# Kernel tuning notes

Hardware: AMD Instinct MI355X
Metric: run time of the kernel (lower is better)

## Reference

```python
import jax, jax.numpy as jnp
import numpy as np

HIDDEN = 3584
N_HEADS = 28
N_KV = 4
HEAD_DIM = HIDDEN // N_HEADS  # 128
BS, SEQ = 4, 2048
EPS = 1e-6
ROPE_THETA = 1000000.0


def setup_inputs() -> dict:
    key = jax.random.key(0)
    ks = jax.random.split(key, 9)
    s = 0.02
    x = jax.random.normal(ks[0], (BS, SEQ, HIDDEN), dtype=jnp.float32)
    positions = jnp.broadcast_to(jnp.arange(SEQ, dtype=jnp.int32), (BS, SEQ))
    ln_w = jnp.ones((HIDDEN,), dtype=jnp.float32)
    Wq = jax.random.normal(ks[1], (N_HEADS * HEAD_DIM, HIDDEN), dtype=jnp.float32) * s
    bq = jax.random.normal(ks[2], (N_HEADS * HEAD_DIM,), dtype=jnp.float32) * s
    Wk = jax.random.normal(ks[3], (N_KV * HEAD_DIM, HIDDEN), dtype=jnp.float32) * s
    bk = jax.random.normal(ks[4], (N_KV * HEAD_DIM,), dtype=jnp.float32) * s
    Wv = jax.random.normal(ks[5], (N_KV * HEAD_DIM, HIDDEN), dtype=jnp.float32) * s
    bv = jax.random.normal(ks[6], (N_KV * HEAD_DIM,), dtype=jnp.float32) * s
    Wo = jax.random.normal(ks[7], (HIDDEN, N_HEADS * HEAD_DIM), dtype=jnp.float32) * s
    return {"x": x, "positions": positions, "ln_w": ln_w, "Wq": Wq, "bq": bq,
            "Wk": Wk, "bk": bk, "Wv": Wv, "bv": bv, "Wo": Wo}


def _rms_norm(x, w, eps):
    var = jnp.mean(x * x, axis=-1, keepdims=True)
    return x * jax.lax.rsqrt(var + eps) * w


def _rope(x, positions):
    # x: [b, s, h, d], neox-style rotary, theta = ROPE_THETA
    d = x.shape[-1]
    inv_freq = 1.0 / (ROPE_THETA ** (jnp.arange(0, d, 2, dtype=jnp.float32) / d))
    ang = positions.astype(jnp.float32)[..., None] * inv_freq  # [b, s, d/2]
    cos = jnp.cos(ang)[:, :, None, :]
    sin = jnp.sin(ang)[:, :, None, :]
    x1, x2 = jnp.split(x, 2, axis=-1)
    return jnp.concatenate([x1 * cos - x2 * sin, x2 * cos + x1 * sin], axis=-1)


def reference(x, positions, ln_w, Wq, bq, Wk, bk, Wv, bv, Wo):
    bs, seq, _ = x.shape
    h = _rms_norm(x, ln_w, EPS)
    q = jnp.einsum('bsh,oh->bso', h, Wq) + bq
    k = jnp.einsum('bsh,oh->bso', h, Wk) + bk
    v = jnp.einsum('bsh,oh->bso', h, Wv) + bv  # computed but unused downstream (as in source)
    q = _rope(q.reshape(bs, seq, N_HEADS, HEAD_DIM), positions)
    k = _rope(k.reshape(bs, seq, N_KV, HEAD_DIM), positions)  # unused downstream (as in source)
    out = jnp.einsum('bso,ho->bsh', q.reshape(bs, seq, -1), Wo) + x
    return out
```

## Files before the change

kernel.cpp:

```cpp
#include <hip/hip_runtime.h>
#include <hip/hip_bf16.h>


#define HIDDEN   3584
#define NQ       3584
#define NTOK     8192
#define NPAIR    64
#define EPSV     1e-6f

typedef __hip_bfloat16 bf16;
typedef __bf16 bf16x8 __attribute__((ext_vector_type(8)));
typedef float  f32x4  __attribute__((ext_vector_type(4)));

static __device__ __forceinline__ unsigned short f2bu(float f) {
  bf16 h = __float2bfloat16(f);
  return __builtin_bit_cast(unsigned short, h);
}
static __device__ __forceinline__ void stv(float* p, float v) { *p = v; }
static __device__ __forceinline__ void stv(bf16* p, float v) { *p = __float2bfloat16(v); }

__global__ __launch_bounds__(256)
void cvt_f32_bf16(const float* __restrict__ s, bf16* __restrict__ d, int n4) {
  int i = blockIdx.x * 256 + threadIdx.x;
  if (i >= n4) return;
  float4 f = ((const float4*)s)[i];
  ushort4 o;
  o.x = f2bu(f.x); o.y = f2bu(f.y); o.z = f2bu(f.z); o.w = f2bu(f.w);
  ((ushort4*)d)[i] = o;
}

__global__ __launch_bounds__(256)
void rmsnorm_k(const float* __restrict__ x, const float* __restrict__ w,
               bf16* __restrict__ h) {
  const int row = blockIdx.x;
  const int t = threadIdx.x;
  const float4* xr = (const float4*)(x + (size_t)row * HIDDEN);
  const float4* wr = (const float4*)w;

  float4 v0 = xr[t], v1 = xr[t + 256], v2 = xr[t + 512];
  float4 v3 = make_float4(0.f, 0.f, 0.f, 0.f);
  if (t < 128) v3 = xr[t + 768];

  float ss = v0.x*v0.x + v0.y*v0.y + v0.z*v0.z + v0.w*v0.w
           + v1.x*v1.x + v1.y*v1.y + v1.z*v1.z + v1.w*v1.w
           + v2.x*v2.x + v2.y*v2.y + v2.z*v2.z + v2.w*v2.w
           + v3.x*v3.x + v3.y*v3.y + v3.z*v3.z + v3.w*v3.w;

#pragma unroll
  for (int off = 32; off > 0; off >>= 1) ss += __shfl_down(ss, off);
  __shared__ float red[4];
  if ((t & 63) == 0) red[t >> 6] = ss;
  __syncthreads();
  float tot = red[0] + red[1] + red[2] + red[3];
  float scale = rsqrtf(tot * (1.0f / HIDDEN) + EPSV);

  ushort4* hr = (ushort4*)(h + (size_t)row * HIDDEN);
  float4 w0 = wr[t], w1 = wr[t + 256], w2 = wr[t + 512];
  ushort4 o;
  o.x = f2bu(v0.x*scale*w0.x); o.y = f2bu(v0.y*scale*w0.y);
  o.z = f2bu(v0.z*scale*w0.z); o.w = f2bu(v0.w*scale*w0.w);
  hr[t] = o;
  o.x = f2bu(v1.x*scale*w1.x); o.y = f2bu(v1.y*scale*w1.y);
  o.z = f2bu(v1.z*scale*w1.z); o.w = f2bu(v1.w*scale*w1.w);
  hr[t + 256] = o;
  o.x = f2bu(v2.x*scale*w2.x); o.y = f2bu(v2.y*scale*w2.y);
  o.z = f2bu(v2.z*scale*w2.z); o.w = f2bu(v2.w*scale*w2.w);
  hr[t + 512] = o;
  if (t < 128) {
    float4 w3 = wr[t + 768];
    o.x = f2bu(v3.x*scale*w3.x); o.y = f2bu(v3.y*scale*w3.y);
    o.z = f2bu(v3.z*scale*w3.z); o.w = f2bu(v3.w*scale*w3.w);
    hr[t + 768] = o;
  }
}

__global__ __launch_bounds__(256)
void rope_tab_k(const int* __restrict__ pos, float2* __restrict__ tab) {
  int idx = blockIdx.x * 256 + threadIdx.x;
  int t = idx >> 6;
  int i = idx & 63;
  float inv = exp2f(-(float)i * (19.931568569324174f / 64.0f));
  float ang = (float)pos[t] * inv;
  float s, c;
  sincosf(ang, &s, &c);
  tab[idx] = make_float2(c, s);
}

__global__ __launch_bounds__(256)
void rope_apply_k(bf16* __restrict__ q, const float2* __restrict__ tab) {
  const int t = blockIdx.x;
  bf16* qt = q + (size_t)t * NQ;
  const float2* tb = tab + (size_t)t * NPAIR;
  for (int j = threadIdx.x; j < 28 * NPAIR; j += 256) {
    int head = j >> 6;
    int i = j & 63;
    float2 cs = tb[i];
    int base = head * 128 + i;
    float x1 = __bfloat162float(qt[base]);
    float x2 = __bfloat162float(qt[base + 64]);
    qt[base]      = __float2bfloat16(x1 * cs.x - x2 * cs.y);
    qt[base + 64] = __float2bfloat16(x2 * cs.x + x1 * cs.y);
  }
}

#define BMT 256
#define BNT 256
#define BKT 64

#define BARRIER() __builtin_amdgcn_s_barrier()
#define VMW(n)    asm volatile("s_waitcnt vmcnt(" #n ")" ::: "memory")

template <int MODE, typename OutT>
__global__ __launch_bounds__(512, 2)
void gemm256(const bf16* __restrict__ A, const bf16* __restrict__ B,
             const float* __restrict__ aux, OutT* __restrict__ C,
             int M, int N, int K) {
  __shared__ __align__(16) bf16 sA[2][BMT][BKT];
  __shared__ __align__(16) bf16 sB[2][BNT][BKT];

  const int tid  = threadIdx.x;
  const int wave = tid >> 6;
  const int lane = tid & 63;
  const int wm   = wave >> 2;
  const int wn   = wave & 3;
  const int fr   = lane & 15;
  const int ks   = lane >> 4;
  const int sx   = fr & 7;

  const int nwg = gridDim.x;
  const int cpx = nwg >> 3;
  const int swz = (blockIdx.x & 7) * cpx + (blockIdx.x >> 3);
  const int gn  = N / BNT;
  const int bm  = (swz / gn) * BMT;
  const int bn  = (swz % gn) * BNT;

  const bf16* Ab = A + (size_t)bm * K;
  const bf16* Bb = B + (size_t)bn * K;

  const int NT = K / BKT;

  const int srw = lane >> 3;
  const int ssl = lane & 7;

  auto stage64 = [&](const bf16* gpanel, int kt, bf16* ldst, int rbase) {
    const int r  = rbase + wave * 8 + srw;
    const int sg = ssl ^ srw;
    const bf16* src = gpanel + (size_t)r * K + (size_t)kt * BKT + sg * 8;
    __builtin_amdgcn_global_load_lds(
        (const __attribute__((address_space(1))) void*)src,
        (__attribute__((address_space(3))) void*)(ldst + (size_t)(wave * 8) * BKT),
        16, 0, 0);
  };
  auto stage16k = [&](int kind, int buf, int kt) {
    if (kt >= NT) return;
    if (kind == 0)      { stage64(Ab, kt, &sA[buf][0][0],   0);   stage64(Ab, kt, &sA[buf][128][0], 128); }
    else if (kind == 1) { stage64(Ab, kt, &sA[buf][64][0],  64);  stage64(Ab, kt, &sA[buf][192][0], 192); }
    else if (kind == 2) { stage64(Bb, kt, &sB[buf][0][0],   0);   stage64(Bb, kt, &sB[buf][64][0],  64); }
    else                { stage64(Bb, kt, &sB[buf][128][0], 128); stage64(Bb, kt, &sB[buf][192][0], 192); }
  };

  f32x4 acc[8][4];
#pragma unroll
  for (int i = 0; i < 8; ++i)
#pragma unroll
    for (int j = 0; j < 4; ++j)
      acc[i][j] = (f32x4){0.f, 0.f, 0.f, 0.f};

  bf16x8 bfr[4][2];
  bf16x8 afr[2][2];

  auto loadA = [&](int buf, int qq) {
#pragma unroll
    for (int i = 0; i < 2; ++i)
#pragma unroll
      for (int kk = 0; kk < 2; ++kk) {
        const int R  = wm * 128 + qq * 32 + i * 16 + fr;
        const int sp = (kk * 4 + ks) ^ sx;
        afr[i][kk] = *(const bf16x8*)&sA[buf][R][sp * 8];
      }
  };
  auto loadB = [&](int buf) {
#pragma unroll
    for (int j = 0; j < 4; ++j)
#pragma unroll
      for (int kk = 0; kk < 2; ++kk) {
        const int R  = wn * 64 + j * 16 + fr;
        const int sp = (kk * 4 + ks) ^ sx;
        bfr[j][kk] = *(const bf16x8*)&sB[buf][R][sp * 8];
      }
  };
  auto domfma = [&](int q) {
#pragma unroll
    for (int i = 0; i < 2; ++i)
#pragma unroll
      for (int j = 0; j < 4; ++j)
#pragma unroll
        for (int kk = 0; kk < 2; ++kk)
          acc[q * 2 + i][j] = __builtin_amdgcn_mfma_f32_16x16x32_bf16(
              afr[i][kk], bfr[j][kk], acc[q * 2 + i][j], 0, 0, 0);
  };

  stage16k(2, 0, 0); stage16k(3, 0, 0); stage16k(0, 0, 0); stage16k(1, 0, 0);
  stage16k(2, 1, 1); stage16k(3, 1, 1); stage16k(0, 1, 1);
  VMW(6);
  BARRIER();

  const int nit = NT / 2;

  for (int it = 0; it < nit; ++it) {
    const bool last = (it == nit - 1);
#pragma unroll
    for (int u = 0; u < 2; ++u) {
#pragma unroll
      for (int q = 0; q < 4; ++q) {
        const int ph = u * 4 + q;
        loadA(u, q);
        if (q == 0) loadB(u);
        if (ph == 0)      stage16k(1, 1, 2 * it + 1);
        else if (ph == 1) stage16k(2, 0, 2 * it + 2);
        else if (ph == 2) stage16k(3, 0, 2 * it + 2);
        else if (ph == 3) stage16k(0, 0, 2 * it + 2);
        else if (ph == 4) stage16k(1, 0, 2 * it + 2);
        else if (ph == 5) stage16k(2, 1, 2 * it + 3);
        else if (ph == 6) stage16k(3, 1, 2 * it + 3);
        else              stage16k(0, 1, 2 * it + 3);
        BARRIER();
        __builtin_amdgcn_s_setprio(1);
        domfma(q);
        __builtin_amdgcn_s_setprio(0);
        if (ph == 3) {
          if (!last) { VMW(6); } else { VMW(2); }
        } else if (ph == 5) {
          if (last)  { VMW(0); }
        } else if (ph == 7) {
          if (!last) { VMW(6); }
        }
        BARRIER();
      }
    }
  }

#pragma unroll
  for (int f = 0; f < 8; ++f) {
    const int rb = bm + wm * 128 + f * 16 + ks * 4;
#pragma unroll
    for (int j = 0; j < 4; ++j) {
      const int col = bn + wn * 64 + j * 16 + fr;
#pragma unroll
      for (int r = 0; r < 4; ++r) {
        const int row = rb + r;
        float v = acc[f][j][r];
        if (MODE == 0) v += aux[col];
        else           v += aux[(size_t)row * N + col];
        stv(&C[(size_t)row * N + col], v);
      }
    }
  }
}

extern "C" void kernel_launch(void* const* d_in, const int* in_sizes, int n_in,
                              void* d_out, int out_size, void* d_ws, size_t ws_size,
                              hipStream_t stream) {
  (void)in_sizes; (void)n_in; (void)out_size; (void)ws_size;
  const float* x    = (const float*)d_in[0];
  const int*   pos  = (const int*)d_in[1];
  const float* ln_w = (const float*)d_in[2];
  const float* Wq   = (const float*)d_in[3];
  const float* bq   = (const float*)d_in[4];
  const float* Wo   = (const float*)d_in[9];
  float* out = (float*)d_out;

  char* ws = (char*)d_ws;
  size_t off = 0;
  bf16* h    = (bf16*)(ws + off); off += (size_t)NTOK * HIDDEN * sizeof(bf16);
  bf16* q    = (bf16*)(ws + off); off += (size_t)NTOK * NQ * sizeof(bf16);
  bf16* Wqb  = (bf16*)(ws + off); off += (size_t)NQ * HIDDEN * sizeof(bf16);
  bf16* Wob  = (bf16*)(ws + off); off += (size_t)HIDDEN * NQ * sizeof(bf16);
  float2* tab = (float2*)(ws + off); off += (size_t)NTOK * NPAIR * sizeof(float2);

  const int n4 = NQ * HIDDEN / 4;
  cvt_f32_bf16<<<(n4 + 255) / 256, 256, 0, stream>>>(Wq, Wqb, n4);
  cvt_f32_bf16<<<(n4 + 255) / 256, 256, 0, stream>>>(Wo, Wob, n4);
  rmsnorm_k<<<NTOK, 256, 0, stream>>>(x, ln_w, h);
  rope_tab_k<<<(NTOK * NPAIR) / 256, 256, 0, stream>>>(pos, tab);

  const int nblk = (NTOK / BMT) * (NQ / BNT);
  gemm256<0, bf16><<<nblk, 512, 0, stream>>>(h, Wqb, bq, q, NTOK, NQ, HIDDEN);
  rope_apply_k<<<NTOK, 256, 0, stream>>>(q, tab);
  gemm256<1, float><<<nblk, 512, 0, stream>>>(q, Wob, x, out, NTOK, HIDDEN, NQ);
}
```

Before: 496.3 us.

## Load GEMM B operand straight from global into double-buffered registers, drop LDS B

Measured after the change: 742.1 us. 49.5% more time.

```diff
diff --git a/kernel.cpp b/kernel.cpp
--- a/kernel.cpp
+++ b/kernel.cpp
@@ -116,7 +116,6 @@
              const float* __restrict__ aux, OutT* __restrict__ C,
              int M, int N, int K) {
   __shared__ __align__(16) bf16 sA[2][BMT][BKT];
-  __shared__ __align__(16) bf16 sB[2][BNT][BKT];
 
   const int tid  = threadIdx.x;
   const int wave = tid >> 6;
@@ -142,22 +141,18 @@
   const int srw = lane >> 3;
   const int ssl = lane & 7;
 
-  auto stage64 = [&](const bf16* gpanel, int kt, bf16* ldst, int rbase) {
+  auto stage64 = [&](int kt, int buf, int rbase) {
+    if (kt >= NT) return;
     const int r  = rbase + wave * 8 + srw;
     const int sg = ssl ^ srw;
-    const bf16* src = gpanel + (size_t)r * K + (size_t)kt * BKT + sg * 8;
+    const bf16* src = Ab + (size_t)r * K + (size_t)kt * BKT + sg * 8;
     __builtin_amdgcn_global_load_lds(
         (const __attribute__((address_space(1))) void*)src,
-        (__attribute__((address_space(3))) void*)(ldst + (size_t)(wave * 8) * BKT),
+        (__attribute__((address_space(3))) void*)(&sA[buf][rbase][0] + (size_t)(wave * 8) * BKT),
         16, 0, 0);
   };
-  auto stage16k = [&](int kind, int buf, int kt) {
-    if (kt >= NT) return;
-    if (kind == 0)      { stage64(Ab, kt, &sA[buf][0][0],   0);   stage64(Ab, kt, &sA[buf][128][0], 128); }
-    else if (kind == 1) { stage64(Ab, kt, &sA[buf][64][0],  64);  stage64(Ab, kt, &sA[buf][192][0], 192); }
-    else if (kind == 2) { stage64(Bb, kt, &sB[buf][0][0],   0);   stage64(Bb, kt, &sB[buf][64][0],  64); }
-    else                { stage64(Bb, kt, &sB[buf][128][0], 128); stage64(Bb, kt, &sB[buf][192][0], 192); }
-  };
+  auto stageAH0 = [&](int kt, int buf) { stage64(kt, buf, 0);  stage64(kt, buf, 128); };
+  auto stageAH1 = [&](int kt, int buf) { stage64(kt, buf, 64); stage64(kt, buf, 192); };
 
   f32x4 acc[8][4];
 #pragma unroll
@@ -166,8 +161,21 @@
     for (int j = 0; j < 4; ++j)
       acc[i][j] = (f32x4){0.f, 0.f, 0.f, 0.f};
 
-  bf16x8 bfr[4][2];
+  bf16x8 bP[4][2], bN[4][2];
   bf16x8 afr[2][2];
+
+  auto loadBg = [&](int kt, bf16x8 (&dst)[4][2]) {
+    if (kt >= NT) return;
+#pragma unroll
+    for (int jf = 0; jf < 4; ++jf)
+#pragma unroll
+      for (int kk = 0; kk < 2; ++kk) {
+        const bf16* src = Bb + (size_t)(wn * 64 + jf * 16 + fr) * K
+                             + (size_t)kt * BKT + kk * 32 + ks * 8;
+        asm volatile("global_load_dwordx4 %0, %1, off"
+                     : "=v"(dst[jf][kk]) : "v"(src) : "memory");
+      }
+  };
 
   auto loadA = [&](int buf, int qq) {
 #pragma unroll
@@ -179,17 +187,7 @@
         afr[i][kk] = *(const bf16x8*)&sA[buf][R][sp * 8];
       }
   };
-  auto loadB = [&](int buf) {
-#pragma unroll
-    for (int j = 0; j < 4; ++j)
-#pragma unroll
-      for (int kk = 0; kk < 2; ++kk) {
-        const int R  = wn * 64 + j * 16 + fr;
-        const int sp = (kk * 4 + ks) ^ sx;
-        bfr[j][kk] = *(const bf16x8*)&sB[buf][R][sp * 8];
-      }
-  };
-  auto domfma = [&](int q) {
+  auto domfma = [&](int q, bf16x8 (&bc)[4][2]) {
 #pragma unroll
     for (int i = 0; i < 2; ++i)
 #pragma unroll
@@ -197,12 +195,13 @@
 #pragma unroll
         for (int kk = 0; kk < 2; ++kk)
           acc[q * 2 + i][j] = __builtin_amdgcn_mfma_f32_16x16x32_bf16(
-              afr[i][kk], bfr[j][kk], acc[q * 2 + i][j], 0, 0, 0);
-  };
-
-  stage16k(2, 0, 0); stage16k(3, 0, 0); stage16k(0, 0, 0); stage16k(1, 0, 0);
-  stage16k(2, 1, 1); stage16k(3, 1, 1); stage16k(0, 1, 1);
-  VMW(6);
+              afr[i][kk], bc[j][kk], acc[q * 2 + i][j], 0, 0, 0);
+  };
+
+  loadBg(0, bP);
+  stageAH0(0, 0); stageAH1(0, 0); stageAH0(1, 1);
+  VMW(2);
+  __builtin_amdgcn_sched_barrier(0);
   BARRIER();
 
   const int nit = NT / 2;
@@ -211,29 +210,22 @@
     const bool last = (it == nit - 1);
 #pragma unroll
     for (int u = 0; u < 2; ++u) {
+      const int kt = 2 * it + u;
 #pragma unroll
       for (int q = 0; q < 4; ++q) {
-        const int ph = u * 4 + q;
         loadA(u, q);
-        if (q == 0) loadB(u);
-        if (ph == 0)      stage16k(1, 1, 2 * it + 1);
-        else if (ph == 1) stage16k(2, 0, 2 * it + 2);
-        else if (ph == 2) stage16k(3, 0, 2 * it + 2);
-        else if (ph == 3) stage16k(0, 0, 2 * it + 2);
-        else if (ph == 4) stage16k(1, 0, 2 * it + 2);
-        else if (ph == 5) stage16k(2, 1, 2 * it + 3);
-        else if (ph == 6) stage16k(3, 1, 2 * it + 3);
-        else              stage16k(0, 1, 2 * it + 3);
+        if (q == 0)      stageAH1(kt + 1, u ^ 1);
+        else if (q == 1) { if (u == 0) loadBg(kt + 1, bN);
+                           else        loadBg(kt + 1, bP); }
+        else if (q == 2) stageAH0(kt + 2, u);
         BARRIER();
         __builtin_amdgcn_s_setprio(1);
-        domfma(q);
+        if (u == 0) domfma(q, bP);
+        else        domfma(q, bN);
         __builtin_amdgcn_s_setprio(0);
-        if (ph == 3) {
-          if (!last) { VMW(6); } else { VMW(2); }
-        } else if (ph == 5) {
-          if (last)  { VMW(0); }
-        } else if (ph == 7) {
-          if (!last) { VMW(6); }
+        if (q == 3) {
+          if (!last) { VMW(2); } else { VMW(0); }
+          __builtin_amdgcn_sched_barrier(0);
         }
         BARRIER();
       }
```

## Shrink GEMM tiles to 128x128 with simpler double-buffered pipeline

Applied to the files above, without the earlier changes.

Result: slower. 595.7 us (+20.0%).

```diff
diff --git a/kernel.cpp b/kernel.cpp
--- a/kernel.cpp
+++ b/kernel.cpp
@@ -103,16 +103,16 @@
   }
 }
 
-#define BMT 256
-#define BNT 256
+#define BMT 128
+#define BNT 128
 #define BKT 64
 
 #define BARRIER() __builtin_amdgcn_s_barrier()
 #define VMW(n)    asm volatile("s_waitcnt vmcnt(" #n ")" ::: "memory")
 
 template <int MODE, typename OutT>
-__global__ __launch_bounds__(512, 2)
-void gemm256(const bf16* __restrict__ A, const bf16* __restrict__ B,
+__global__ __launch_bounds__(512, 4)
+void gemm128(const bf16* __restrict__ A, const bf16* __restrict__ B,
              const float* __restrict__ aux, OutT* __restrict__ C,
              int M, int N, int K) {
   __shared__ __align__(16) bf16 sA[2][BMT][BKT];
@@ -143,116 +143,105 @@
   const int ssl = lane & 7;
 
   auto stage64 = [&](const bf16* gpanel, int kt, bf16* ldst, int rbase) {
+    if (kt >= NT) return;
     const int r  = rbase + wave * 8 + srw;
     const int sg = ssl ^ srw;
     const bf16* src = gpanel + (size_t)r * K + (size_t)kt * BKT + sg * 8;
     __builtin_amdgcn_global_load_lds(
         (const __attribute__((address_space(1))) void*)src,
-        (__attribute__((address_space(3))) void*)(ldst + (size_t)(wave * 8) * BKT),
+        (__attribute__((address_space(3))) void*)(ldst + (size_t)(rbase + wave * 8) * BKT),
         16, 0, 0);
   };
-  auto stage16k = [&](int kind, int buf, int kt) {
-    if (kt >= NT) return;
-    if (kind == 0)      { stage64(Ab, kt, &sA[buf][0][0],   0);   stage64(Ab, kt, &sA[buf][128][0], 128); }
-    else if (kind == 1) { stage64(Ab, kt, &sA[buf][64][0],  64);  stage64(Ab, kt, &sA[buf][192][0], 192); }
-    else if (kind == 2) { stage64(Bb, kt, &sB[buf][0][0],   0);   stage64(Bb, kt, &sB[buf][64][0],  64); }
-    else                { stage64(Bb, kt, &sB[buf][128][0], 128); stage64(Bb, kt, &sB[buf][192][0], 192); }
-  };
-
-  f32x4 acc[8][4];
-#pragma unroll
-  for (int i = 0; i < 8; ++i)
-#pragma unroll
-    for (int j = 0; j < 4; ++j)
+
+  f32x4 acc[4][2];
+#pragma unroll
+  for (int i = 0; i < 4; ++i)
+#pragma unroll
+    for (int j = 0; j < 2; ++j)
       acc[i][j] = (f32x4){0.f, 0.f, 0.f, 0.f};
 
-  bf16x8 bfr[4][2];
+  bf16x8 bfr[2][2];
   bf16x8 afr[2][2];
 
-  auto loadA = [&](int buf, int qq) {
+  auto loadA = [&](int buf, int half) {
 #pragma unroll
     for (int i = 0; i < 2; ++i)
 #pragma unroll
       for (int kk = 0; kk < 2; ++kk) {
-        const int R  = wm * 128 + qq * 32 + i * 16 + fr;
+        const int R  = half * 64 + wm * 32 + i * 16 + fr;
         const int sp = (kk * 4 + ks) ^ sx;
         afr[i][kk] = *(const bf16x8*)&sA[buf][R][sp * 8];
       }
   };
   auto loadB = [&](int buf) {
 #pragma unroll
-    for (int j = 0; j < 4; ++j)
+    for (int j = 0; j < 2; ++j)
 #pragma unroll
       for (int kk = 0; kk < 2; ++kk) {
-        const int R  = wn * 64 + j * 16 + fr;
+        const int R  = wn * 32 + j * 16 + fr;
         const int sp = (kk * 4 + ks) ^ sx;
         bfr[j][kk] = *(const bf16x8*)&sB[buf][R][sp * 8];
       }
   };
-  auto domfma = [&](int q) {
+  auto domfma = [&](int half) {
 #pragma unroll
     for (int i = 0; i < 2; ++i)
 #pragma unroll
-      for (int j = 0; j < 4; ++j)
+      for (int j = 0; j < 2; ++j)
 #pragma unroll
         for (int kk = 0; kk < 2; ++kk)
-          acc[q * 2 + i][j] = __builtin_amdgcn_mfma_f32_16x16x32_bf16(
-              afr[i][kk], bfr[j][kk], acc[q * 2 + i][j], 0, 0, 0);
-  };
-
-  stage16k(2, 0, 0); stage16k(3, 0, 0); stage16k(0, 0, 0); stage16k(1, 0, 0);
-  stage16k(2, 1, 1); stage16k(3, 1, 1); stage16k(0, 1, 1);
-  VMW(6);
+          acc[half * 2 + i][j] = __builtin_amdgcn_mfma_f32_16x16x32_bf16(
+              afr[i][kk], bfr[j][kk], acc[half * 2 + i][j], 0, 0, 0);
+  };
+
+  stage64(Bb, 0, &sB[0][0][0], 0);  stage64(Bb, 0, &sB[0][0][0], 64);
+  stage64(Ab, 0, &sA[0][0][0], 0);  stage64(Ab, 0, &sA[0][0][0], 64);
+  VMW(0);
   BARRIER();
 
-  const int nit = NT / 2;
-
-  for (int it = 0; it < nit; ++it) {
-    const bool last = (it == nit - 1);
+  for (int it = 0; it < NT / 2; ++it) {
 #pragma unroll
     for (int u = 0; u < 2; ++u) {
-#pragma unroll
-      for (int q = 0; q < 4; ++q) {
-        const int ph = u * 4 + q;
-        loadA(u, q);
-        if (q == 0) loadB(u);
-        if (ph == 0)      stage16k(1, 1, 2 * it + 1);
-        else if (ph == 1) stage16k(2, 0, 2 * it + 2);
-        else if (ph == 2) stage16k(3, 0, 2 * it + 2);
-        else if (ph == 3) stage16k(0, 0, 2 * it + 2);
-        else if (ph == 4) stage16k(1, 0, 2 * it + 2);
-        else if (ph == 5) stage16k(2, 1, 2 * it + 3);
-        else if (ph == 6) stage16k(3, 1, 2 * it + 3);
-        else              stage16k(0, 1, 2 * it + 3);
-        BARRIER();
-        __builtin_amdgcn_s_setprio(1);
-        domfma(q);
-        __builtin_amdgcn_s_setprio(0);
-        if (ph == 3) {
-          if (!last) { VMW(6); } else { VMW(2); }
-        } else if (ph == 5) {
-          if (last)  { VMW(0); }
-        } else if (ph == 7) {
-          if (!last) { VMW(6); }
+      const int kt = 2 * it + u;
+      const bool lastt = (kt == NT - 1);
+      loadA(u, 0);
+      loadB(u);
+      stage64(Bb, kt + 1, &sB[u ^ 1][0][0], 0);
+      stage64(Bb, kt + 1, &sB[u ^ 1][0][0], 64);
+      stage64(Ab, kt + 1, &sA[u ^ 1][0][0], 0);
+      BARRIER();
+      __builtin_amdgcn_s_setprio(1);
+      domfma(0);
+      __builtin_amdgcn_s_setprio(0);
+      if (lastt) { VMW(0); } else { VMW(3); }
+      BARRIER();
+      loadA(u, 1);
+      stage64(Ab, kt + 1, &sA[u ^ 1][0][0], 64);
+      BARRIER();
+      __builtin_amdgcn_s_setprio(1);
+      domfma(1);
+      __builtin_amdgcn_s_setprio(0);
+      if (lastt) { VMW(0); } else { VMW(1); }
+      BARRIER();
+    }
+  }
+
+#pragma unroll
+  for (int half = 0; half < 2; ++half) {
+#pragma unroll
+    for (int i = 0; i < 2; ++i) {
+      const int rb = bm + half * 64 + wm * 32 + i * 16 + ks * 4;
+#pragma unroll
+      for (int j = 0; j < 2; ++j) {
+        const int col = bn + wn * 32 + j * 16 + fr;
+#pragma unroll
+        for (int r = 0; r < 4; ++r) {
+          const int row = rb + r;
+          float v = acc[half * 2 + i][j][r];
+          if (MODE == 0) v += aux[col];
+          else           v += aux[(size_t)row * N + col];
+          stv(&C[(size_t)row * N + col], v);
         }
-        BARRIER();
-      }
-    }
-  }
-
-#pragma unroll
-  for (int f = 0; f < 8; ++f) {
-    const int rb = bm + wm * 128 + f * 16 + ks * 4;
-#pragma unroll
-    for (int j = 0; j < 4; ++j) {
-      const int col = bn + wn * 64 + j * 16 + fr;
-#pragma unroll
-      for (int r = 0; r < 4; ++r) {
-        const int row = rb + r;
-        float v = acc[f][j][r];
-        if (MODE == 0) v += aux[col];
-        else           v += aux[(size_t)row * N + col];
-        stv(&C[(size_t)row * N + col], v);
       }
     }
   }
@@ -285,7 +274,7 @@
   rope_tab_k<<<(NTOK * NPAIR) / 256, 256, 0, stream>>>(pos, tab);
 
   const int nblk = (NTOK / BMT) * (NQ / BNT);
-  gemm256<0, bf16><<<nblk, 512, 0, stream>>>(h, Wqb, bq, q, NTOK, NQ, HIDDEN);
+  gemm128<0, bf16><<<nblk, 512, 0, stream>>>(h, Wqb, bq, q, NTOK, NQ, HIDDEN);
   rope_apply_k<<<NTOK, 256, 0, stream>>>(q, tab);
-  gemm256<1, float><<<nblk, 512, 0, stream>>>(q, Wob, x, out, NTOK, HIDDEN, NQ);
-}
+  gemm128<1, float><<<nblk, 512, 0, stream>>>(q, Wob, x, out, NTOK, HIDDEN, NQ);
+}
```

## Fuse RoPE into Q-projection GEMM epilogue and merge weight conversions

Applied to the files above, without the earlier changes.

New measurement: 485.5 us. 2.2% less time.

```diff
diff --git a/kernel.cpp b/kernel.cpp
--- a/kernel.cpp
+++ b/kernel.cpp
@@ -20,9 +20,13 @@
 static __device__ __forceinline__ void stv(bf16* p, float v) { *p = __float2bfloat16(v); }
 
 __global__ __launch_bounds__(256)
-void cvt_f32_bf16(const float* __restrict__ s, bf16* __restrict__ d, int n4) {
+void cvt2_f32_bf16(const float* __restrict__ s1, bf16* __restrict__ d1,
+                   const float* __restrict__ s2, bf16* __restrict__ d2, int n4) {
   int i = blockIdx.x * 256 + threadIdx.x;
-  if (i >= n4) return;
+  const float* s; bf16* d;
+  if (i < n4)           { s = s1; d = d1; }
+  else if (i < 2 * n4)  { s = s2; d = d2; i -= n4; }
+  else return;
   float4 f = ((const float4*)s)[i];
   ushort4 o;
   o.x = f2bu(f.x); o.y = f2bu(f.y); o.z = f2bu(f.z); o.w = f2bu(f.w);
@@ -86,23 +90,6 @@
   tab[idx] = make_float2(c, s);
 }
 
-__global__ __launch_bounds__(256)
-void rope_apply_k(bf16* __restrict__ q, const float2* __restrict__ tab) {
-  const int t = blockIdx.x;
-  bf16* qt = q + (size_t)t * NQ;
-  const float2* tb = tab + (size_t)t * NPAIR;
-  for (int j = threadIdx.x; j < 28 * NPAIR; j += 256) {
-    int head = j >> 6;
-    int i = j & 63;
-    float2 cs = tb[i];
-    int base = head * 128 + i;
-    float x1 = __bfloat162float(qt[base]);
-    float x2 = __bfloat162float(qt[base + 64]);
-    qt[base]      = __float2bfloat16(x1 * cs.x - x2 * cs.y);
-    qt[base + 64] = __float2bfloat16(x2 * cs.x + x1 * cs.y);
-  }
-}
-
 #define BMT 256
 #define BNT 256
 #define BKT 64
@@ -113,8 +100,8 @@
 template <int MODE, typename OutT>
 __global__ __launch_bounds__(512, 2)
 void gemm256(const bf16* __restrict__ A, const bf16* __restrict__ B,
-             const float* __restrict__ aux, OutT* __restrict__ C,
-             int M, int N, int K) {
+             const float* __restrict__ aux, const float2* __restrict__ tab,
+             OutT* __restrict__ C, int M, int N, int K) {
   __shared__ __align__(16) bf16 sA[2][BMT][BKT];
   __shared__ __align__(16) bf16 sB[2][BNT][BKT];
 
@@ -127,6 +114,10 @@
   const int ks   = lane >> 4;
   const int sx   = fr & 7;
 
+  auto nmap = [&](int j) {
+    return (wn >> 1) * 128 + (wn & 1) * 32 + ((j & 1) << 4) + ((j >> 1) << 6);
+  };
+
   const int nwg = gridDim.x;
   const int cpx = nwg >> 3;
   const int swz = (blockIdx.x & 7) * cpx + (blockIdx.x >> 3);
@@ -184,7 +175,7 @@
     for (int j = 0; j < 4; ++j)
 #pragma unroll
       for (int kk = 0; kk < 2; ++kk) {
-        const int R  = wn * 64 + j * 16 + fr;
+        const int R  = nmap(j) + fr;
         const int sp = (kk * 4 + ks) ^ sx;
         bfr[j][kk] = *(const bf16x8*)&sB[buf][R][sp * 8];
       }
@@ -240,19 +231,40 @@
     }
   }
 
-#pragma unroll
-  for (int f = 0; f < 8; ++f) {
-    const int rb = bm + wm * 128 + f * 16 + ks * 4;
-#pragma unroll
-    for (int j = 0; j < 4; ++j) {
-      const int col = bn + wn * 64 + j * 16 + fr;
-#pragma unroll
-      for (int r = 0; r < 4; ++r) {
-        const int row = rb + r;
-        float v = acc[f][j][r];
-        if (MODE == 0) v += aux[col];
-        else           v += aux[(size_t)row * N + col];
-        stv(&C[(size_t)row * N + col], v);
+  if (MODE == 0) {
+#pragma unroll
+    for (int f = 0; f < 8; ++f) {
+      const int rb = bm + wm * 128 + f * 16 + ks * 4;
+#pragma unroll
+      for (int j = 0; j < 2; ++j) {
+        const int i_idx = (wn & 1) * 32 + j * 16 + fr;
+        const int c1 = bn + nmap(j) + fr;
+        const int c2 = c1 + 64;
+        const float b1 = aux[c1], b2 = aux[c2];
+#pragma unroll
+        for (int r = 0; r < 4; ++r) {
+          const int row = rb + r;
+          const float2 cs = tab[(size_t)row * NPAIR + i_idx];
+          const float x1 = acc[f][j][r]     + b1;
+          const float x2 = acc[f][j + 2][r] + b2;
+          stv(&C[(size_t)row * N + c1], x1 * cs.x - x2 * cs.y);
+          stv(&C[(size_t)row * N + c2], x2 * cs.x + x1 * cs.y);
+        }
+      }
+    }
+  } else {
+#pragma unroll
+    for (int f = 0; f < 8; ++f) {
+      const int rb = bm + wm * 128 + f * 16 + ks * 4;
+#pragma unroll
+      for (int j = 0; j < 4; ++j) {
+        const int col = bn + nmap(j) + fr;
+#pragma unroll
+        for (int r = 0; r < 4; ++r) {
+          const int row = rb + r;
+          stv(&C[(size_t)row * N + col],
+              acc[f][j][r] + aux[(size_t)row * N + col]);
+        }
       }
     }
   }
@@ -279,13 +291,11 @@
   float2* tab = (float2*)(ws + off); off += (size_t)NTOK * NPAIR * sizeof(float2);
 
   const int n4 = NQ * HIDDEN / 4;
-  cvt_f32_bf16<<<(n4 + 255) / 256, 256, 0, stream>>>(Wq, Wqb, n4);
-  cvt_f32_bf16<<<(n4 + 255) / 256, 256, 0, stream>>>(Wo, Wob, n4);
+  cvt2_f32_bf16<<<(2 * n4 + 255) / 256, 256, 0, stream>>>(Wq, Wqb, Wo, Wob, n4);
   rmsnorm_k<<<NTOK, 256, 0, stream>>>(x, ln_w, h);
   rope_tab_k<<<(NTOK * NPAIR) / 256, 256, 0, stream>>>(pos, tab);
 
   const int nblk = (NTOK / BMT) * (NQ / BNT);
-  gemm256<0, bf16><<<nblk, 512, 0, stream>>>(h, Wqb, bq, q, NTOK, NQ, HIDDEN);
-  rope_apply_k<<<NTOK, 256, 0, stream>>>(q, tab);
-  gemm256<1, float><<<nblk, 512, 0, stream>>>(q, Wob, x, out, NTOK, HIDDEN, NQ);
-}
+  gemm256<0, bf16><<<nblk, 512, 0, stream>>>(h, Wqb, bq, tab, q, NTOK, NQ, HIDDEN);
+  gemm256<1, float><<<nblk, 512, 0, stream>>>(q, Wob, x, nullptr, out, NTOK, HIDDEN, NQ);
+}
```
